# Performance work log

Hardware: AMD Instinct MI355X
Metric: run time of the kernel (lower is better)

## Reference

```python
import jax, jax.numpy as jnp
import numpy as np
from math import sqrt

N = 40000      # nodes
E = 640000     # edges
DIN = 128
H = 128
DOUT = 128
L = 3          # n_layers
TAU = 1.0
MIN_NORM = 1e-15
BN_EPS = 1e-5


def _norm(v):
    return jnp.linalg.norm(v, axis=-1, keepdims=True)


def reflect_at_zero(x, mu):
    # a = reflection_center(mu); isometric_transform(x, a)
    a = mu / jnp.maximum(jnp.sum(mu * mu, -1, keepdims=True), MIN_NORM)
    r2 = jnp.sum(a * a, -1, keepdims=True) - 1.0
    u = x - a
    return r2 / jnp.maximum(jnp.sum(u * u, -1, keepdims=True), MIN_NORM) * u + a


def reflect_through_zero(p, q, x):
    p_ = p / jnp.maximum(_norm(p), MIN_NORM)
    q_ = q / jnp.maximum(_norm(q), MIN_NORM)
    r = q_ - p_
    m = jnp.sum(r * x, -1, keepdims=True) / jnp.sum(r * r, -1, keepdims=True)
    return x - 2.0 * r * m


def logmap0(y):
    yn = jnp.maximum(_norm(y), MIN_NORM)
    return y / yn * jnp.arctanh(jnp.clip(yn, -1.0 + 1e-15, 1.0 - 1e-15))


def gin_layer(x, src, dst, w1, b1, g, bt, w2, b2):
    # GINConv(eps=0, sum aggregation): mlp(x + sum_{j->i} x_j)
    agg = jax.ops.segment_sum(x[src], dst, num_segments=N)  # [N,H]
    h = x + agg
    h = jax.nn.relu(h @ w1.T + b1)
    mu = jnp.mean(h, axis=0)
    var = jnp.mean((h - mu) ** 2, axis=0)  # biased var (BatchNorm training stats)
    h = (h - mu) / jnp.sqrt(var + BN_EPS) * g + bt
    h = jax.nn.relu(h @ w2.T + b2)
    return h


def setup_inputs() -> dict:
    key = jax.random.key(0)
    ks = jax.random.split(key, 16)
    s = 0.05
    x = jax.random.normal(ks[0], (N, DIN), jnp.float32)
    edge_index = jax.random.randint(ks[1], (2, E), 0, N, dtype=jnp.int64)
    fc0_w = jax.random.normal(ks[2], (H, DIN), jnp.float32) * s
    fc0_b = jax.random.normal(ks[3], (H,), jnp.float32) * s
    w1 = jax.random.normal(ks[4], (L, H, H), jnp.float32) * s
    b1 = jax.random.normal(ks[5], (L, H), jnp.float32) * s
    gamma = jnp.ones((L, H), jnp.float32)
    beta = jnp.zeros((L, H), jnp.float32)
    w2 = jax.random.normal(ks[6], (L, H, H), jnp.float32) * s
    b2 = jax.random.normal(ks[7], (L, H), jnp.float32) * s
    fc_out_w = jax.random.normal(ks[8], (DOUT, H), jnp.float32) * s
    fc_out_b = jax.random.normal(ks[9], (DOUT,), jnp.float32) * s
    p = (-1.0 / sqrt(H)) * jnp.ones((H,), jnp.float32)
    return {"x": x, "edge_index": edge_index, "fc0_w": fc0_w, "fc0_b": fc0_b,
            "w1": w1, "b1": b1, "gamma": gamma, "beta": beta, "w2": w2, "b2": b2,
            "fc_out_w": fc_out_w, "fc_out_b": fc_out_b, "p": p}


def reference(x, edge_index, fc0_w, fc0_b, w1, b1, gamma, beta, w2, b2, fc_out_w, fc_out_b, p):
    # With continuous random features every row is unique, so torch.unique(dim=0)
    # is a pure permutation (counts==1) and the unique/scatter_add/gather pipeline
    # collapses to per-node tree embeddings; the final index_select undoes the perm.
    scaling = jnp.tanh(jnp.asarray(TAU, jnp.float32) / 2.0)
    src, dst = edge_index[0], edge_index[1]
    h = jax.nn.relu(x @ fc0_w.T + fc0_b)                 # [N,H]
    hd = jax.lax.stop_gradient(h)                        # unique under no_grad
    z_prev = jnp.zeros((N, H), h.dtype)                  # level-0 root embedding
    z_cur = scaling * hd / _norm(hd)                     # level-1 embedding
    for i in range(L):
        h = gin_layer(h, src, dst, w1[i], b1[i], gamma[i], beta[i], w2[i], b2[i])
        hd = jax.lax.stop_gradient(h)
        z_ch = scaling * hd / _norm(hd)
        z_par = reflect_at_zero(z_prev, z_cur)
        z_ch = reflect_through_zero(z_par, p, z_ch)
        z_all = reflect_at_zero(z_ch, z_cur)
        z_prev, z_cur = z_cur, z_all
    xh = logmap0(z_cur)                                  # [N,H] tangent space
    out = xh @ fc_out_w.T + fc_out_b                     # [N,DOUT]
    return out / jnp.maximum(_norm(out), 1e-12)          # F.normalize
```

## Files before the change

### kernel.cpp

```cpp
#include <hip/hip_runtime.h>
#include <math.h>

#define NN 40000
#define HD 128
#define NE 640000
#define MINN 1e-15f
#define NSB 157
#define GB  2500
#define HB_BLK 512

typedef __attribute__((ext_vector_type(8))) short bf16x8;
typedef __attribute__((ext_vector_type(4))) float f32x4;

__device__ __forceinline__ float red16(float v){
  v += __shfl_xor(v, 1, 64); v += __shfl_xor(v, 2, 64);
  v += __shfl_xor(v, 4, 64); v += __shfl_xor(v, 8, 64);
  return v;
}

__device__ __forceinline__ float bf2f(short h){
  return __uint_as_float(((unsigned)(unsigned short)h) << 16);
}
__device__ __forceinline__ short f2bf(float v){
  unsigned u = __float_as_uint(v);
  u += 0x7FFF + ((u >> 16) & 1);
  return (short)(u >> 16);
}

#define GACC(A,V) \
  A[0] += __uint_as_float((V).x << 16); A[1] += __uint_as_float((V).x & 0xffff0000u); \
  A[2] += __uint_as_float((V).y << 16); A[3] += __uint_as_float((V).y & 0xffff0000u); \
  A[4] += __uint_as_float((V).z << 16); A[5] += __uint_as_float((V).z & 0xffff0000u); \
  A[6] += __uint_as_float((V).w << 16); A[7] += __uint_as_float((V).w & 0xffff0000u);

__device__ __forceinline__ void loadA_g(const float* __restrict__ A, long rb,
                                        int l15, int kg, float av[4][8]){
  #pragma unroll
  for (int ks = 0; ks < 4; ++ks){
    const float* ap = A + (rb + l15)*HD + ks*32 + kg*8;
    float4 a0 = *(const float4*)ap;
    float4 a1 = *(const float4*)(ap + 4);
    av[ks][0]=a0.x; av[ks][1]=a0.y; av[ks][2]=a0.z; av[ks][3]=a0.w;
    av[ks][4]=a1.x; av[ks][5]=a1.y; av[ks][6]=a1.z; av[ks][7]=a1.w;
  }
}

__device__ __forceinline__ void mfma_core(const float av[4][8],
    const bf16x8* __restrict__ bh, const bf16x8* __restrict__ bl,
    int lane, f32x4 acc[8]){
  #pragma unroll
  for (int ct = 0; ct < 8; ++ct){
    acc[ct][0]=0.f; acc[ct][1]=0.f; acc[ct][2]=0.f; acc[ct][3]=0.f;
  }
  #pragma unroll
  for (int ks = 0; ks < 4; ++ks){
    bf16x8 ah, al;
    #pragma unroll
    for (int j = 0; j < 8; ++j){
      float v = av[ks][j];
      short hh = f2bf(v);
      short ll = f2bf(v - bf2f(hh));
      ah[j] = hh; al[j] = ll;
    }
    #pragma unroll
    for (int ct = 0; ct < 8; ++ct){
      bf16x8 bhv = bh[(ks*8 + ct)*64 + lane];
      bf16x8 blv = bl[(ks*8 + ct)*64 + lane];
      acc[ct] = __builtin_amdgcn_mfma_f32_16x16x32_bf16(ah, bhv, acc[ct], 0, 0, 0);
      acc[ct] = __builtin_amdgcn_mfma_f32_16x16x32_bf16(al, bhv, acc[ct], 0, 0, 0);
      acc[ct] = __builtin_amdgcn_mfma_f32_16x16x32_bf16(ah, blv, acc[ct], 0, 0, 0);
    }
  }
}

__device__ __forceinline__ void biasrelu(f32x4 acc[8], const float* __restrict__ bias,
                                         int l15, bool relu){
  #pragma unroll
  for (int ct = 0; ct < 8; ++ct){
    float bb = bias[ct*16 + l15];
    #pragma unroll
    for (int q = 0; q < 4; ++q){
      float v = acc[ct][q] + bb;
      if (relu) v = fmaxf(v, 0.f);
      acc[ct][q] = v;
    }
  }
}

__global__ __launch_bounds__(64) void zero_prep_k(const float* __restrict__ fc0_w,
    const float* __restrict__ w1, const float* __restrict__ w2,
    const float* __restrict__ fco_w, bf16x8* __restrict__ bhi,
    bf16x8* __restrict__ blo, int* __restrict__ cnt, float* __restrict__ part2){
  int bid = blockIdx.x;
  if (bid < 256){
    int gid = bid*64 + threadIdx.x;
    int widx = gid >> 11;
    const float* W;
    if (widx == 0)      W = fc0_w;
    else if (widx <= 3) W = w1 + (size_t)(widx-1)*HD*HD;
    else if (widx <= 6) W = w2 + (size_t)(widx-4)*HD*HD;
    else                W = fco_w;
    int f  = gid & 2047;
    int ln = f & 63;
    int ct = (f >> 6) & 7;
    int ks = f >> 9;
    int n  = ct*16 + (ln & 15);
    int k0 = ks*32 + (ln >> 4)*8;
    bf16x8 hv, lv;
    #pragma unroll
    for (int j = 0; j < 8; ++j){
      float v = W[n*HD + k0 + j];
      short hh = f2bf(v);
      short ll = f2bf(v - bf2f(hh));
      hv[j] = hh; lv[j] = ll;
    }
    bhi[widx*2048 + f] = hv; blo[widx*2048 + f] = lv;
  } else {
    int i = (bid-256)*64 + threadIdx.x;
    const int st = 161*64;
    for (int j = i; j < NN; j += st) cnt[j] = 0;
    for (int j = i; j < 2048; j += st) part2[j] = 0.f;
  }
}

__global__ __launch_bounds__(64) void fc0hist_k(const float* __restrict__ x,
    const int* __restrict__ dst, int* __restrict__ cnt,
    const bf16x8* __restrict__ bhi, const bf16x8* __restrict__ blo,
    const float* __restrict__ fc0_b, float* __restrict__ h,
    unsigned short* __restrict__ hb, float* __restrict__ zB, float scaling){
  int bid = blockIdx.x;
  if (bid >= GB){
    int i = (bid - GB)*64 + threadIdx.x;
    const int st = HB_BLK*64;
    for (; i < NE; i += st) atomicAdd(&cnt[dst[i]], 1);
    return;
  }
  const int lane = threadIdx.x;
  const int l15 = lane & 15, kg = lane >> 4;
  const long rb = (long)bid*16;
  float av[4][8]; loadA_g(x, rb, l15, kg, av);
  f32x4 acc[8]; mfma_core(av, bhi, blo, lane, acc);
  biasrelu(acc, fc0_b, l15, true);
  #pragma unroll
  for (int ct = 0; ct < 8; ++ct)
    #pragma unroll
    for (int q = 0; q < 4; ++q){
      float v = acc[ct][q];
      long row = rb + kg*4 + q;
      h[row*HD + ct*16 + l15] = v;
      hb[row*HD + ct*16 + l15] = (unsigned short)f2bf(v);
    }
  #pragma unroll
  for (int q = 0; q < 4; ++q){
    float ss = 0.f;
    #pragma unroll
    for (int ct = 0; ct < 8; ++ct) ss = fmaf(acc[ct][q], acc[ct][q], ss);
    ss = red16(ss);
    float sc2 = scaling / sqrtf(ss);
    long row = rb + kg*4 + q;
    #pragma unroll
    for (int ct = 0; ct < 8; ++ct)
      zB[row*HD + ct*16 + l15] = acc[ct][q]*sc2;
  }
}

__global__ __launch_bounds__(256) void scan1_k(const int* __restrict__ cnt,
    int* __restrict__ locpre, int* __restrict__ btot){
  __shared__ int s[256];
  int t = threadIdx.x;
  int idx = blockIdx.x*256 + t;
  int v = (idx < NN) ? cnt[idx] : 0;
  s[t] = v; __syncthreads();
  for (int off = 1; off < 256; off <<= 1){
    int x = (t >= off) ? s[t-off] : 0;
    __syncthreads(); s[t] += x; __syncthreads();
  }
  locpre[idx] = s[t] - v;
  if (t == 255) btot[blockIdx.x] = s[255];
}

__global__ __launch_bounds__(256) void scan23_k(const int* __restrict__ btot,
    const int* __restrict__ locpre, int* __restrict__ ptr, int* __restrict__ fil){
  __shared__ int s[256];
  int t = threadIdx.x;
  int v = (t < NSB) ? btot[t] : 0;
  s[t] = v; __syncthreads();
  for (int off = 1; off < 256; off <<= 1){
    int x = (t >= off) ? s[t-off] : 0;
    __syncthreads(); s[t] += x; __syncthreads();
  }
  int bid = blockIdx.x;
  int pre = (bid == 0) ? 0 : s[bid-1];
  int idx = bid*256 + t;
  if (idx < NN){
    int v2 = pre + locpre[idx];
    ptr[idx] = v2; fil[idx] = v2;
  }
  if (bid == 0 && t == 0) ptr[NN] = s[NSB-1];
}

__global__ void fill_k(const int* __restrict__ src, const int* __restrict__ dst,
    int* __restrict__ fill, unsigned short* __restrict__ eidx, int ne){
  int i = blockIdx.x*blockDim.x + threadIdx.x;
  int st = gridDim.x*blockDim.x;
  for (; i < ne; i += st){
    int d = dst[i];
    int pos = atomicAdd(&fill[d], 1);
    eidx[pos] = (unsigned short)src[i];
  }
}

__global__ __launch_bounds__(256) void gw1_k(const float* __restrict__ h,
    const bf16x8* __restrict__ bhi, const bf16x8* __restrict__ blo,
    const float* __restrict__ bias, float* __restrict__ t,
    float* __restrict__ part2, const uint4* __restrict__ hb4,
    const int* __restrict__ gptr, const unsigned short* __restrict__ eidx)
{
  __shared__ float tl[16*132];
  const int tid = threadIdx.x;
  const int lane = tid & 63;
  const int wv = tid >> 6;
  const int l15 = lane & 15, kg = lane >> 4;
  const long rb = (long)blockIdx.x*16;

  {
    const int r = wv*4 + kg;
    const long node = rb + r;
    int beg = gptr[node], end = gptr[node+1];
    const float4* selfp = (const float4*)(h + node*HD) + l15*2;
    float4 s0 = selfp[0], s1 = selfp[1];
    float ga[8] = {s0.x,s0.y,s0.z,s0.w,s1.x,s1.y,s1.z,s1.w};
    int e = beg;
    for (; e + 8 <= end; e += 8){
      int i0 = eidx[e],   i1 = eidx[e+1], i2 = eidx[e+2], i3 = eidx[e+3];
      int i4 = eidx[e+4], i5 = eidx[e+5], i6 = eidx[e+6], i7 = eidx[e+7];
      uint4 v0 = hb4[(long)i0*16 + l15];
      uint4 v1 = hb4[(long)i1*16 + l15];
      uint4 v2 = hb4[(long)i2*16 + l15];
      uint4 v3 = hb4[(long)i3*16 + l15];
      uint4 v4 = hb4[(long)i4*16 + l15];
      uint4 v5 = hb4[(long)i5*16 + l15];
      uint4 v6 = hb4[(long)i6*16 + l15];
      uint4 v7 = hb4[(long)i7*16 + l15];
      GACC(ga,v0) GACC(ga,v1) GACC(ga,v2) GACC(ga,v3)
      GACC(ga,v4) GACC(ga,v5) GACC(ga,v6) GACC(ga,v7)
    }
    if (e + 4 <= end){
      int i0 = eidx[e], i1 = eidx[e+1], i2 = eidx[e+2], i3 = eidx[e+3];
      uint4 v0 = hb4[(long)i0*16 + l15];
      uint4 v1 = hb4[(long)i1*16 + l15];
      uint4 v2 = hb4[(long)i2*16 + l15];
      uint4 v3 = hb4[(long)i3*16 + l15];
      GACC(ga,v0) GACC(ga,v1) GACC(ga,v2) GACC(ga,v3)
      e += 4;
    }
    for (; e < end; ++e){
      uint4 v = hb4[(long)eidx[e]*16 + l15];
      GACC(ga,v)
    }
    float4* tp = (float4*)(tl + r*132 + l15*8);
    float4 o0 = {ga[0],ga[1],ga[2],ga[3]};
    float4 o1 = {ga[4],ga[5],ga[6],ga[7]};
    tp[0] = o0; tp[1] = o1;
  }
  __syncthreads();
  if (wv != 0) return;

  float av[4][8];
  #pragma unroll
  for (int ks = 0; ks < 4; ++ks){
    const float* ap = tl + l15*132 + ks*32 + kg*8;
    float4 a0 = *(const float4*)ap;
    float4 a1 = *(const float4*)(ap + 4);
    av[ks][0]=a0.x; av[ks][1]=a0.y; av[ks][2]=a0.z; av[ks][3]=a0.w;
    av[ks][4]=a1.x; av[ks][5]=a1.y; av[ks][6]=a1.z; av[ks][7]=a1.w;
  }
  f32x4 acc[8]; mfma_core(av, bhi, blo, lane, acc);
  biasrelu(acc, bias, l15, true);

  #pragma unroll
  for (int ct = 0; ct < 8; ++ct){
    float s = 0.f, q2 = 0.f;
    #pragma unroll
    for (int q = 0; q < 4; ++q){
      float v = acc[ct][q];
      s += v; q2 = fmaf(v, v, q2);
    }
    s  += __shfl_xor(s, 16, 64);  s  += __shfl_xor(s, 32, 64);
    q2 += __shfl_xor(q2, 16, 64); q2 += __shfl_xor(q2, 32, 64);
    if (kg == 0){
      const int slot = (blockIdx.x & 7)*256;
      atomicAdd(&part2[slot + ct*16 + l15], s);
      atomicAdd(&part2[slot + 128 + ct*16 + l15], q2);
    }
  }

  #pragma unroll
  for (int ct = 0; ct < 8; ++ct)
    #pragma unroll
    for (int q = 0; q < 4; ++q)
      t[(rb + kg*4 + q)*HD + ct*16 + l15] = acc[ct][q];
}

template<bool RELU, bool BN_IN, bool XH_IN, bool NORM_OUT,
         bool WRITE_HB, bool WRITE_OUT, bool ZSTEP, bool ZFIRST, bool FUSEOUT>
__global__ __launch_bounds__(64) void mgemm_k(const float* __restrict__ A,
    const bf16x8* __restrict__ bhi, const bf16x8* __restrict__ blo,
    const float* __restrict__ bias, const float* __restrict__ scale,
    const float* __restrict__ shift, float* __restrict__ out,
    unsigned short* __restrict__ hbout, float* __restrict__ zout, float scaling,
    const float* __restrict__ zpin, const float* __restrict__ zcin,
    const float* __restrict__ pvec,
    const bf16x8* __restrict__ bhi2, const bf16x8* __restrict__ blo2,
    const float* __restrict__ bias2, float* __restrict__ out2)
{
  __shared__ float tl[FUSEOUT ? 16*132 : 1];
  const int lane = threadIdx.x;
  const int l15 = lane & 15, kg = lane >> 4;
  const long rb = (long)blockIdx.x*16;

  float av[4][8];
  loadA_g(A, rb, l15, kg, av);

  float zc_a[4][8], zp_a[4][8], pvr[8];
  if constexpr (ZSTEP){
    #pragma unroll
    for (int q = 0; q < 4; ++q){
      const long row = rb + kg*4 + q;
      #pragma unroll
      for (int ct = 0; ct < 8; ++ct)
        zc_a[q][ct] = zcin[row*HD + ct*16 + l15];
    }
    if constexpr (!ZFIRST){
      #pragma unroll
      for (int q = 0; q < 4; ++q){
        const long row = rb + kg*4 + q;
        #pragma unroll
        for (int ct = 0; ct < 8; ++ct)
          zp_a[q][ct] = zpin[row*HD + ct*16 + l15];
      }
    }
    #pragma unroll
    for (int ct = 0; ct < 8; ++ct) pvr[ct] = pvec[ct*16 + l15];
  }

  if (BN_IN){
    #pragma unroll
    for (int ks = 0; ks < 4; ++ks){
      const int k0 = ks*32 + kg*8;
      float4 s0 = *(const float4*)(scale + k0);
      float4 s1 = *(const float4*)(scale + k0 + 4);
      float4 h0 = *(const float4*)(shift + k0);
      float4 h1 = *(const float4*)(shift + k0 + 4);
      float sc[8] = {s0.x,s0.y,s0.z,s0.w,s1.x,s1.y,s1.z,s1.w};
      float sh[8] = {h0.x,h0.y,h0.z,h0.w,h1.x,h1.y,h1.z,h1.w};
      #pragma unroll
      for (int j = 0; j < 8; ++j)
        av[ks][j] = fmaf(av[ks][j], sc[j], sh[j]);
    }
  }
  if (XH_IN){
    float ss = 0.f;
    #pragma unroll
    for (int ks = 0; ks < 4; ++ks)
      #pragma unroll
      for (int j = 0; j < 8; ++j)
        ss = fmaf(av[ks][j], av[ks][j], ss);
    ss += __shfl_xor(ss, 16, 64);
    ss += __shfl_xor(ss, 32, 64);
    float n = sqrtf(ss);
    float yn = fmaxf(n, MINN);
    float c = fminf(yn, 1.0f);
    float at = 0.5f*logf((1.0f + c)/(1.0f - c));
    float scx = at / yn;
    #pragma unroll
    for (int ks = 0; ks < 4; ++ks)
      #pragma unroll
      for (int j = 0; j < 8; ++j)
        av[ks][j] *= scx;
  }

  f32x4 acc[8];
  mfma_core(av, bhi, blo, lane, acc);
  biasrelu(acc, bias, l15, RELU);

  if (NORM_OUT){
    float ss[4] = {0.f,0.f,0.f,0.f};
    #pragma unroll
    for (int ct = 0; ct < 8; ++ct)
      #pragma unroll
      for (int q = 0; q < 4; ++q)
        ss[q] = fmaf(acc[ct][q], acc[ct][q], ss[q]);
    #pragma unroll
    for (int q = 0; q < 4; ++q){
      #pragma unroll
      for (int m = 1; m < 16; m <<= 1) ss[q] += __shfl_xor(ss[q], m, 64);
      ss[q] = 1.0f / fmaxf(sqrtf(ss[q]), 1e-12f);
    }
    #pragma unroll
    for (int ct = 0; ct < 8; ++ct)
      #pragma unroll
      for (int q = 0; q < 4; ++q)
        acc[ct][q] *= ss[q];
  }

  if constexpr (ZSTEP){
    float pq = 0.f;
    #pragma unroll
    for (int ct = 0; ct < 8; ++ct) pq = fmaf(pvr[ct], pvr[ct], pq);
    pq = red16(pq);
    float qi = 1.0f / fmaxf(sqrtf(pq), MINN);
    #pragma unroll
    for (int ct = 0; ct < 8; ++ct) pvr[ct] *= qi;

    #pragma unroll
    for (int q = 0; q < 4; ++q){
      const long row = rb + kg*4 + q;
      float zc[8], zp[8];
      #pragma unroll
      for (int ct = 0; ct < 8; ++ct) zc[ct] = zc_a[q][ct];
      if constexpr (!ZFIRST){
        #pragma unroll
        for (int ct = 0; ct < 8; ++ct) zp[ct] = zp_a[q][ct];
      } else {
        #pragma unroll
        for (int ct = 0; ct < 8; ++ct) zp[ct] = 0.f;
      }
      float hh = 0.f, cc = 0.f;
      #pragma unroll
      for (int ct = 0; ct < 8; ++ct){
        hh = fmaf(acc[ct][q], acc[ct][q], hh);
        cc = fmaf(zc[ct], zc[ct], cc);
      }
      hh = red16(hh); cc = red16(cc);
      float zs = scaling / sqrtf(hh);
      float di = 1.0f / fmaxf(cc, MINN);
      float r2 = cc*di*di - 1.0f;
      float a[8], u[8]; float uu = 0.f;
      #pragma unroll
      for (int ct = 0; ct < 8; ++ct){
        a[ct] = zc[ct]*di;
        u[ct] = zp[ct] - a[ct];
        uu = fmaf(u[ct], u[ct], uu);
      }
      uu = red16(uu);
      float f = r2 / fmaxf(uu, MINN);
      float zpar[8]; float pn2 = 0.f;
      #pragma unroll
      for (int ct = 0; ct < 8; ++ct){
        zpar[ct] = fmaf(f, u[ct], a[ct]);
        pn2 = fmaf(zpar[ct], zpar[ct], pn2);
      }
      pn2 = red16(pn2);
      float pinv = 1.0f / fmaxf(sqrtf(pn2), MINN);
      float rv[8], zch[8]; float rz = 0.f, rr = 0.f;
      #pragma unroll
      for (int ct = 0; ct < 8; ++ct){
        zch[ct] = acc[ct][q]*zs;
        rv[ct] = pvr[ct] - zpar[ct]*pinv;
        rz = fmaf(rv[ct], zch[ct], rz);
        rr = fmaf(rv[ct], rv[ct], rr);
      }
      rz = red16(rz); rr = red16(rr);
      float mm = rz / rr;
      float u2[8]; float uu2 = 0.f;
      #pragma unroll
      for (int ct = 0; ct < 8; ++ct){
        float z2 = fmaf(-2.0f*mm, rv[ct], zch[ct]);
        u2[ct] = z2 - a[ct];
        uu2 = fmaf(u2[ct], u2[ct], uu2);
      }
      uu2 = red16(uu2);
      float f2 = r2 / fmaxf(uu2, MINN);
      if constexpr (FUSEOUT){
        #pragma unroll
        for (int ct = 0; ct < 8; ++ct)
          tl[(kg*4 + q)*132 + ct*16 + l15] = fmaf(f2, u2[ct], a[ct]);
      } else {
        #pragma unroll
        for (int ct = 0; ct < 8; ++ct)
          zout[row*HD + ct*16 + l15] = fmaf(f2, u2[ct], a[ct]);
      }
    }
  }

  if constexpr (FUSEOUT){
    float av2[4][8];
    #pragma unroll
    for (int ks = 0; ks < 4; ++ks){
      const float* ap = tl + l15*132 + ks*32 + kg*8;
      float4 a0 = *(const float4*)ap;
      float4 a1 = *(const float4*)(ap + 4);
      av2[ks][0]=a0.x; av2[ks][1]=a0.y; av2[ks][2]=a0.z; av2[ks][3]=a0.w;
      av2[ks][4]=a1.x; av2[ks][5]=a1.y; av2[ks][6]=a1.z; av2[ks][7]=a1.w;
    }
    float ss = 0.f;
    #pragma unroll
    for (int ks = 0; ks < 4; ++ks)
      #pragma unroll
      for (int j = 0; j < 8; ++j)
        ss = fmaf(av2[ks][j], av2[ks][j], ss);
    ss += __shfl_xor(ss, 16, 64);
    ss += __shfl_xor(ss, 32, 64);
    float n = sqrtf(ss);
    float yn = fmaxf(n, MINN);
    float c = fminf(yn, 1.0f);
    float at = 0.5f*logf((1.0f + c)/(1.0f - c));
    float scx = at / yn;
    #pragma unroll
    for (int ks = 0; ks < 4; ++ks)
      #pragma unroll
      for (int j = 0; j < 8; ++j)
        av2[ks][j] *= scx;

    f32x4 acc2[8];
    mfma_core(av2, bhi2, blo2, lane, acc2);
    biasrelu(acc2, bias2, l15, false);

    float ss4[4] = {0.f,0.f,0.f,0.f};
    #pragma unroll
    for (int ct = 0; ct < 8; ++ct)
      #pragma unroll
      for (int q = 0; q < 4; ++q)
        ss4[q] = fmaf(acc2[ct][q], acc2[ct][q], ss4[q]);
    #pragma unroll
    for (int q = 0; q < 4; ++q){
      #pragma unroll
      for (int m = 1; m < 16; m <<= 1) ss4[q] += __shfl_xor(ss4[q], m, 64);
      ss4[q] = 1.0f / fmaxf(sqrtf(ss4[q]), 1e-12f);
    }
    #pragma unroll
    for (int ct = 0; ct < 8; ++ct)
      #pragma unroll
      for (int q = 0; q < 4; ++q)
        out2[(rb + kg*4 + q)*HD + ct*16 + l15] = acc2[ct][q]*ss4[q];
  }

  if constexpr (WRITE_OUT || WRITE_HB){
    #pragma unroll
    for (int ct = 0; ct < 8; ++ct)
      #pragma unroll
      for (int q = 0; q < 4; ++q){
        float v = acc[ct][q];
        long row = rb + kg*4 + q;
        if (WRITE_OUT) out[row*HD + ct*16 + l15] = v;
        if (WRITE_HB) hbout[row*HD + ct*16 + l15] = (unsigned short)f2bf(v);
      }
  }
}

__global__ __launch_bounds__(256) void bnfin_k(float* __restrict__ part2,
    const float* __restrict__ g, const float* __restrict__ b,
    float* __restrict__ scale, float* __restrict__ shift){
  __shared__ float sm[256];
  float tot = 0.f;
  #pragma unroll
  for (int r = 0; r < 8; ++r) tot += part2[r*256 + threadIdx.x];
  sm[threadIdx.x] = tot;
  __syncthreads();
  if (threadIdx.x < 128){
    int c = threadIdx.x;
    float s = sm[c], q = sm[c + 128];
    float mu  = s * (1.0f/NN);
    float var = q * (1.0f/NN) - mu*mu;
    float istd = rsqrtf(var + 1e-5f);
    float scv = g[c]*istd;
    scale[c] = scv;
    shift[c] = fmaf(-mu, scv, b[c]);
  }
  #pragma unroll
  for (int r = 0; r < 8; ++r) part2[r*256 + threadIdx.x] = 0.f;
}

extern "C" void kernel_launch(void* const* d_in, const int* in_sizes, int n_in,
                              void* d_out, int out_size, void* d_ws, size_t ws_size,
                              hipStream_t stream) {
  const float* x       = (const float*)d_in[0];
  const int*   ei      = (const int*)  d_in[1];
  const float* fc0_w   = (const float*)d_in[2];
  const float* fc0_b   = (const float*)d_in[3];
  const float* w1      = (const float*)d_in[4];
  const float* b1      = (const float*)d_in[5];
  const float* gamma   = (const float*)d_in[6];
  const float* beta    = (const float*)d_in[7];
  const float* w2      = (const float*)d_in[8];
  const float* b2      = (const float*)d_in[9];
  const float* fco_w   = (const float*)d_in[10];
  const float* fco_b   = (const float*)d_in[11];
  const float* p       = (const float*)d_in[12];

  float* out = (float*)d_out;
  float* ws  = (float*)d_ws;

  float* h     = ws;
  float* zA    = h   + (size_t)NN*HD;
  float* zB    = zA  + (size_t)NN*HD;
  float* part2 = zB  + (size_t)NN*HD;
  float* scale = part2 + 8*256;
  float* shift = scale + 128;
  bf16x8* bhi  = (bf16x8*)(shift + 128);
  bf16x8* blo  = bhi + 8*2048;
  unsigned short* hb = (unsigned short*)(blo + 8*2048);
  int* cnt     = (int*)(hb + (size_t)NN*HD);
  int* ptr     = cnt + NN;
  int* fil     = ptr + NN + 1;
  unsigned short* eidx = (unsigned short*)(fil + NN);
  int* locpre  = (int*)(eidx + NE);
  int* btot    = locpre + NSB*256;
  float* t = out;

  const int* src = ei;
  const int* dst = ei + NE;
  const float scaling = tanhf(0.5f);

  zero_prep_k<<<417, 64, 0, stream>>>(fc0_w, w1, w2, fco_w, bhi, blo, cnt, part2);

  fc0hist_k<<<GB + HB_BLK, 64, 0, stream>>>(x, dst, cnt, bhi, blo, fc0_b,
                                            h, hb, zB, scaling);

  scan1_k<<<NSB, 256, 0, stream>>>(cnt, locpre, btot);
  scan23_k<<<NSB, 256, 0, stream>>>(btot, locpre, ptr, fil);
  fill_k<<<512, 256, 0, stream>>>(src, dst, fil, eidx, NE);

  float* zprev = zA; float* zcur = zB;

  for (int i = 0; i < 3; ++i) {
    gw1_k<<<GB, 256, 0, stream>>>(
        h, bhi + (1+i)*2048, blo + (1+i)*2048, b1 + i*HD, t, part2,
        (const uint4*)hb, ptr, eidx);
    bnfin_k<<<1, 256, 0, stream>>>(part2, gamma + i*HD, beta + i*HD, scale, shift);
    if (i == 0)
      mgemm_k<true,true,false,false,true,true,true,true,false>
          <<<GB, 64, 0, stream>>>(
          t, bhi + 4*2048, blo + 4*2048, b2, scale, shift, h, hb,
          zprev, scaling, zprev, zcur, p, nullptr, nullptr, nullptr, nullptr);
    else if (i == 1)
      mgemm_k<true,true,false,false,true,true,true,false,false>
          <<<GB, 64, 0, stream>>>(
          t, bhi + 5*2048, blo + 5*2048, b2 + HD, scale, shift, h, hb,
          zprev, scaling, zprev, zcur, p, nullptr, nullptr, nullptr, nullptr);
    else
      mgemm_k<true,true,false,false,false,false,true,false,true>
          <<<GB, 64, 0, stream>>>(
          t, bhi + 6*2048, blo + 6*2048, b2 + 2*HD, scale, shift, nullptr, nullptr,
          nullptr, scaling, zprev, zcur, p,
          bhi + 7*2048, blo + 7*2048, fco_b, out);
    float* tmp = zprev; zprev = zcur; zcur = tmp;
  }
}
```

Before: 295.3 us.

## Split gather across two half-groups and fold BN finalize into last block

```diff
diff --git a/kernel.cpp b/kernel.cpp
--- a/kernel.cpp
+++ b/kernel.cpp
@@ -90,7 +90,8 @@
 __global__ __launch_bounds__(64) void zero_prep_k(const float* __restrict__ fc0_w,
     const float* __restrict__ w1, const float* __restrict__ w2,
     const float* __restrict__ fco_w, bf16x8* __restrict__ bhi,
-    bf16x8* __restrict__ blo, int* __restrict__ cnt, float* __restrict__ part2){
+    bf16x8* __restrict__ blo, int* __restrict__ cnt, float* __restrict__ part2,
+    int* __restrict__ done){
   int bid = blockIdx.x;
   if (bid < 256){
     int gid = bid*64 + threadIdx.x;
@@ -119,7 +120,8 @@
     int i = (bid-256)*64 + threadIdx.x;
     const int st = 161*64;
     for (int j = i; j < NN; j += st) cnt[j] = 0;
-    for (int j = i; j < 2048; j += st) part2[j] = 0.f;
+    for (int j = i; j < 3*2048; j += st) part2[j] = 0.f;
+    if (i < 3) done[i] = 0;
   }
 }
 
@@ -210,13 +212,15 @@
   }
 }
 
-__global__ __launch_bounds__(256) void gw1_k(const float* __restrict__ h,
+__global__ __launch_bounds__(512) void gw1_k(const float* __restrict__ h,
     const bf16x8* __restrict__ bhi, const bf16x8* __restrict__ blo,
     const float* __restrict__ bias, float* __restrict__ t,
     float* __restrict__ part2, const uint4* __restrict__ hb4,
-    const int* __restrict__ gptr, const unsigned short* __restrict__ eidx)
+    const int* __restrict__ gptr, const unsigned short* __restrict__ eidx,
+    const float* __restrict__ gam, const float* __restrict__ bet,
+    float* __restrict__ scale, float* __restrict__ shift, int* __restrict__ done)
 {
-  __shared__ float tl[16*132];
+  __shared__ float tl[2*16*132];
   const int tid = threadIdx.x;
   const int lane = tid & 63;
   const int wv = tid >> 6;
@@ -224,41 +228,50 @@
   const long rb = (long)blockIdx.x*16;
 
   {
-    const int r = wv*4 + kg;
+    const int g = tid >> 4;
+    const int r = g & 15;
+    const int half = g >> 4;
+    const int l = tid & 15;
     const long node = rb + r;
     int beg = gptr[node], end = gptr[node+1];
-    const float4* selfp = (const float4*)(h + node*HD) + l15*2;
-    float4 s0 = selfp[0], s1 = selfp[1];
-    float ga[8] = {s0.x,s0.y,s0.z,s0.w,s1.x,s1.y,s1.z,s1.w};
-    int e = beg;
-    for (; e + 8 <= end; e += 8){
+    int mid = beg + ((end - beg) >> 1);
+    int e  = half ? mid : beg;
+    int e1 = half ? end : mid;
+    float ga[8] = {0.f,0.f,0.f,0.f,0.f,0.f,0.f,0.f};
+    if (!half){
+      const float4* selfp = (const float4*)(h + node*HD) + l*2;
+      float4 s0 = selfp[0], s1 = selfp[1];
+      ga[0]=s0.x; ga[1]=s0.y; ga[2]=s0.z; ga[3]=s0.w;
+      ga[4]=s1.x; ga[5]=s1.y; ga[6]=s1.z; ga[7]=s1.w;
+    }
+    for (; e + 8 <= e1; e += 8){
       int i0 = eidx[e],   i1 = eidx[e+1], i2 = eidx[e+2], i3 = eidx[e+3];
       int i4 = eidx[e+4], i5 = eidx[e+5], i6 = eidx[e+6], i7 = eidx[e+7];
-      uint4 v0 = hb4[(long)i0*16 + l15];
-      uint4 v1 = hb4[(long)i1*16 + l15];
-      uint4 v2 = hb4[(long)i2*16 + l15];
-      uint4 v3 = hb4[(long)i3*16 + l15];
-      uint4 v4 = hb4[(long)i4*16 + l15];
-      uint4 v5 = hb4[(long)i5*16 + l15];
-      uint4 v6 = hb4[(long)i6*16 + l15];
-      uint4 v7 = hb4[(long)i7*16 + l15];
+      uint4 v0 = hb4[(long)i0*16 + l];
+      uint4 v1 = hb4[(long)i1*16 + l];
+      uint4 v2 = hb4[(long)i2*16 + l];
+      uint4 v3 = hb4[(long)i3*16 + l];
+      uint4 v4 = hb4[(long)i4*16 + l];
+      uint4 v5 = hb4[(long)i5*16 + l];
+      uint4 v6 = hb4[(long)i6*16 + l];
+      uint4 v7 = hb4[(long)i7*16 + l];
       GACC(ga,v0) GACC(ga,v1) GACC(ga,v2) GACC(ga,v3)
       GACC(ga,v4) GACC(ga,v5) GACC(ga,v6) GACC(ga,v7)
     }
-    if (e + 4 <= end){
+    if (e + 4 <= e1){
       int i0 = eidx[e], i1 = eidx[e+1], i2 = eidx[e+2], i3 = eidx[e+3];
-      uint4 v0 = hb4[(long)i0*16 + l15];
-      uint4 v1 = hb4[(long)i1*16 + l15];
-      uint4 v2 = hb4[(long)i2*16 + l15];
-      uint4 v3 = hb4[(long)i3*16 + l15];
+      uint4 v0 = hb4[(long)i0*16 + l];
+      uint4 v1 = hb4[(long)i1*16 + l];
+      uint4 v2 = hb4[(long)i2*16 + l];
+      uint4 v3 = hb4[(long)i3*16 + l];
       GACC(ga,v0) GACC(ga,v1) GACC(ga,v2) GACC(ga,v3)
       e += 4;
     }
-    for (; e < end; ++e){
-      uint4 v = hb4[(long)eidx[e]*16 + l15];
+    for (; e < e1; ++e){
+      uint4 v = hb4[(long)eidx[e]*16 + l];
       GACC(ga,v)
     }
-    float4* tp = (float4*)(tl + r*132 + l15*8);
+    float4* tp = (float4*)(tl + half*2112 + r*132 + l*8);
     float4 o0 = {ga[0],ga[1],ga[2],ga[3]};
     float4 o1 = {ga[4],ga[5],ga[6],ga[7]};
     tp[0] = o0; tp[1] = o1;
@@ -272,11 +285,19 @@
     const float* ap = tl + l15*132 + ks*32 + kg*8;
     float4 a0 = *(const float4*)ap;
     float4 a1 = *(const float4*)(ap + 4);
-    av[ks][0]=a0.x; av[ks][1]=a0.y; av[ks][2]=a0.z; av[ks][3]=a0.w;
-    av[ks][4]=a1.x; av[ks][5]=a1.y; av[ks][6]=a1.z; av[ks][7]=a1.w;
+    float4 b0 = *(const float4*)(ap + 2112);
+    float4 b1 = *(const float4*)(ap + 2112 + 4);
+    av[ks][0]=a0.x+b0.x; av[ks][1]=a0.y+b0.y; av[ks][2]=a0.z+b0.z; av[ks][3]=a0.w+b0.w;
+    av[ks][4]=a1.x+b1.x; av[ks][5]=a1.y+b1.y; av[ks][6]=a1.z+b1.z; av[ks][7]=a1.w+b1.w;
   }
   f32x4 acc[8]; mfma_core(av, bhi, blo, lane, acc);
   biasrelu(acc, bias, l15, true);
+
+  #pragma unroll
+  for (int ct = 0; ct < 8; ++ct)
+    #pragma unroll
+    for (int q = 0; q < 4; ++q)
+      t[(rb + kg*4 + q)*HD + ct*16 + l15] = acc[ct][q];
 
   #pragma unroll
   for (int ct = 0; ct < 8; ++ct){
@@ -295,11 +316,29 @@
     }
   }
 
-  #pragma unroll
-  for (int ct = 0; ct < 8; ++ct)
-    #pragma unroll
-    for (int q = 0; q < 4; ++q)
-      t[(rb + kg*4 + q)*HD + ct*16 + l15] = acc[ct][q];
+  __threadfence();
+  int last = 0;
+  if (lane == 0){
+    int v = atomicAdd(done, 1);
+    last = (v == GB - 1) ? 1 : 0;
+  }
+  last = __shfl(last, 0, 64);
+  if (last){
+    for (int c = lane; c < 128; c += 64){
+      float s = 0.f, q = 0.f;
+      #pragma unroll
+      for (int rr = 0; rr < 8; ++rr){
+        s += atomicAdd(&part2[rr*256 + c], 0.0f);
+        q += atomicAdd(&part2[rr*256 + 128 + c], 0.0f);
+      }
+      float mu  = s * (1.0f/NN);
+      float var = q * (1.0f/NN) - mu*mu;
+      float istd = rsqrtf(var + 1e-5f);
+      float scv = gam[c]*istd;
+      scale[c] = scv;
+      shift[c] = fmaf(-mu, scv, bet[c]);
+    }
+  }
 }
 
 template<bool RELU, bool BN_IN, bool XH_IN, bool NORM_OUT,
@@ -549,29 +588,6 @@
   }
 }
 
-__global__ __launch_bounds__(256) void bnfin_k(float* __restrict__ part2,
-    const float* __restrict__ g, const float* __restrict__ b,
-    float* __restrict__ scale, float* __restrict__ shift){
-  __shared__ float sm[256];
-  float tot = 0.f;
-  #pragma unroll
-  for (int r = 0; r < 8; ++r) tot += part2[r*256 + threadIdx.x];
-  sm[threadIdx.x] = tot;
-  __syncthreads();
-  if (threadIdx.x < 128){
-    int c = threadIdx.x;
-    float s = sm[c], q = sm[c + 128];
-    float mu  = s * (1.0f/NN);
-    float var = q * (1.0f/NN) - mu*mu;
-    float istd = rsqrtf(var + 1e-5f);
-    float scv = g[c]*istd;
-    scale[c] = scv;
-    shift[c] = fmaf(-mu, scv, b[c]);
-  }
-  #pragma unroll
-  for (int r = 0; r < 8; ++r) part2[r*256 + threadIdx.x] = 0.f;
-}
-
 extern "C" void kernel_launch(void* const* d_in, const int* in_sizes, int n_in,
                               void* d_out, int out_size, void* d_ws, size_t ws_size,
                               hipStream_t stream) {
@@ -596,9 +612,10 @@
   float* zA    = h   + (size_t)NN*HD;
   float* zB    = zA  + (size_t)NN*HD;
   float* part2 = zB  + (size_t)NN*HD;
-  float* scale = part2 + 8*256;
+  float* scale = part2 + 3*2048;
   float* shift = scale + 128;
-  bf16x8* bhi  = (bf16x8*)(shift + 128);
+  int*   done  = (int*)(shift + 128);
+  bf16x8* bhi  = (bf16x8*)(done + 64);
   bf16x8* blo  = bhi + 8*2048;
   unsigned short* hb = (unsigned short*)(blo + 8*2048);
   int* cnt     = (int*)(hb + (size_t)NN*HD);
@@ -613,7 +630,8 @@
   const int* dst = ei + NE;
   const float scaling = tanhf(0.5f);
 
-  zero_prep_k<<<417, 64, 0, stream>>>(fc0_w, w1, w2, fco_w, bhi, blo, cnt, part2);
+  zero_prep_k<<<417, 64, 0, stream>>>(fc0_w, w1, w2, fco_w, bhi, blo, cnt,
+                                      part2, done);
 
   fc0hist_k<<<GB + HB_BLK, 64, 0, stream>>>(x, dst, cnt, bhi, blo, fc0_b,
                                             h, hb, zB, scaling);
@@ -625,10 +643,10 @@
   float* zprev = zA; float* zcur = zB;
 
   for (int i = 0; i < 3; ++i) {
-    gw1_k<<<GB, 256, 0, stream>>>(
-        h, bhi + (1+i)*2048, blo + (1+i)*2048, b1 + i*HD, t, part2,
-        (const uint4*)hb, ptr, eidx);
-    bnfin_k<<<1, 256, 0, stream>>>(part2, gamma + i*HD, beta + i*HD, scale, shift);
+    gw1_k<<<GB, 512, 0, stream>>>(
+        h, bhi + (1+i)*2048, blo + (1+i)*2048, b1 + i*HD, t, part2 + i*2048,
+        (const uint4*)hb, ptr, eidx, gamma + i*HD, beta + i*HD,
+        scale, shift, done + i);
     if (i == 0)
       mgemm_k<true,true,false,false,true,true,true,true,false>
           <<<GB, 64, 0, stream>>>(
```

New measurement: 510.7 us. +72.9%, slower.
